# Kernel optimization log

Measured on AMD Instinct MI355X. Metric: run time of the kernel, lower is better.

The kernel has to match this reference:

```python
import jax, jax.numpy as jnp
import numpy as np

B, L, DIM, K = 2, 512, 128, 32
EPS = 1e-5  # torch LayerNorm default


def setup_inputs() -> dict:
    key = jax.random.key(0)
    ks = jax.random.split(key, 4)
    s = 1.0 / np.sqrt(DIM)
    s2 = 1.0 / np.sqrt(2 * DIM)
    return {
        "pair_repr": jax.random.normal(ks[0], (B, L, L, DIM), jnp.float32),
        "W_out": jax.random.uniform(ks[1], (DIM, DIM), jnp.float32, -s, s),
        "b_out": jnp.zeros((DIM,), jnp.float32),
        "W_in": jax.random.uniform(ks[2], (DIM, DIM), jnp.float32, -s, s),
        "b_in": jnp.zeros((DIM,), jnp.float32),
        "W_g": jax.random.uniform(ks[3], (2 * DIM, DIM), jnp.float32, -s2, s2),
        "b_g": jnp.zeros((DIM,), jnp.float32),
        "ln_w": jnp.ones((DIM,), jnp.float32),
        "ln_b": jnp.zeros((DIM,), jnp.float32),
    }


def reference(pair_repr, W_out, b_out, W_in, b_in, W_g, b_g, ln_w, ln_b):
    # Eval-mode deterministic sampling: torch.linspace(0, L-1, K).long()
    idx = jnp.floor(jnp.linspace(0.0, L - 1, K)).astype(jnp.int32)

    # Linear is affine, so mean(Linear(x)) == Linear(mean(x)); project after mean.
    out_mean = pair_repr[:, :, idx, :].mean(axis=2)          # (B, L, dim)
    out_agg = out_mean @ W_out + b_out                        # (B, L, dim)
    in_mean = pair_repr[:, idx, :, :].mean(axis=1)            # (B, L, dim)
    in_agg = in_mean @ W_in + b_in                            # (B, L, dim)

    # gate = sigmoid(Linear(cat(out_b, in_b))): split W_g to avoid materializing the 2*dim concat
    Wg_o, Wg_i = W_g[:DIM], W_g[DIM:]
    gate = jax.nn.sigmoid(
        (out_agg @ Wg_o)[:, :, None, :]
        + (in_agg @ Wg_i)[:, None, :, :]
        + b_g
    )                                                         # (B, L, L, dim)

    update = out_agg[:, :, None, :] + in_agg[:, None, :, :]   # (B, L, L, dim)
    x = pair_repr + gate * (update - pair_repr)

    # LayerNorm over last axis (biased variance, matching torch)
    mu = x.mean(axis=-1, keepdims=True)
    var = x.var(axis=-1, keepdims=True)
    return (x - mu) / jnp.sqrt(var + EPS) * ln_w + ln_b
```

## Files before the change

### kernel.cpp

```cpp
#include <hip/hip_runtime.h>
#include <hip/hip_bf16.h>

#define BB 2
#define LL 512
#define DIM 128
#define KK 32
#define EPSF 1e-5f

__global__ __launch_bounds__(DIM) void agg_gemm_kernel(
    const float* __restrict__ pair,
    const float* __restrict__ W_out, const float* __restrict__ b_out,
    const float* __restrict__ W_in,  const float* __restrict__ b_in,
    const float* __restrict__ W_g,
    float* __restrict__ agg,
    float* __restrict__ gpart)
{
    const int t    = threadIdx.x;
    const int bid  = blockIdx.x;
    const int path = bid >> 10;
    const int r    = bid & 1023;
    const int b    = r >> 9;
    const int q    = r & 511;

    __shared__ float sm[DIM];

    const float* base;
    long stride;
    if (path == 0) {
        base   = pair + ((long)(b * LL + q) * LL) * DIM + t;
        stride = DIM;
    } else {
        base   = pair + ((long)b * LL * LL) * DIM + (long)q * DIM + t;
        stride = (long)LL * DIM;
    }
    float acc = 0.f;
#pragma unroll
    for (int k = 0; k < KK; ++k) {
        const int jj = (k * (LL - 1)) / (KK - 1);
        acc += base[(long)jj * stride];
    }
    sm[t] = acc * (1.0f / KK);
    __syncthreads();

    const float* W    = (path == 0) ? W_out : W_in;
    const float* bias = (path == 0) ? b_out : b_in;
    float a = bias[t];
#pragma unroll 8
    for (int k = 0; k < DIM; ++k)
        a += sm[k] * W[k * DIM + t];
    __syncthreads();
    sm[t] = a;
    agg[(long)path * BB * LL * DIM + (long)r * DIM + t] = a;
    __syncthreads();

    const float* Wg = W_g + path * DIM * DIM;
    float g = 0.f;
#pragma unroll 8
    for (int k = 0; k < DIM; ++k)
        g += sm[k] * Wg[k * DIM + t];
    gpart[(long)path * BB * LL * DIM + (long)r * DIM + t] = g;
}

__device__ __forceinline__ void load8(const float* p, float* f) {
    const float4 a = reinterpret_cast<const float4*>(p)[0];
    const float4 b = reinterpret_cast<const float4*>(p)[1];
    f[0] = a.x; f[1] = a.y; f[2] = a.z; f[3] = a.w;
    f[4] = b.x; f[5] = b.y; f[6] = b.z; f[7] = b.w;
}

__global__ __launch_bounds__(256) void fuse_ln_kernel(
    const float* __restrict__ pair,
    const float* __restrict__ out_agg, const float* __restrict__ in_agg,
    const float* __restrict__ go,      const float* __restrict__ gi,
    const float* __restrict__ b_g, const float* __restrict__ ln_w,
    const float* __restrict__ ln_b,
    float* __restrict__ out)
{
    const int  tid    = threadIdx.x;
    const int  lane16 = tid & 15;
    const int  rloc   = tid >> 4;
    const long row    = (long)blockIdx.x * 16 + rloc;
    const int  j      = (int)(row & (LL - 1));
    const long bi     = row >> 9;
    const int  b      = (int)(bi >> 9);
    const int  e0     = lane16 * 8;
    const long bj     = (long)b * LL + j;

    float p[8], gof[8], gif[8], oaf[8], iaf[8], bg[8], lw[8], lb[8];
    load8(pair    + row * DIM + e0, p);
    load8(go      + bi  * DIM + e0, gof);
    load8(gi      + bj  * DIM + e0, gif);
    load8(out_agg + bi  * DIM + e0, oaf);
    load8(in_agg  + bj  * DIM + e0, iaf);
    load8(b_g  + e0, bg);
    load8(ln_w + e0, lw);
    load8(ln_b + e0, lb);

    float x[8];
    float sum = 0.f, ss = 0.f;
#pragma unroll
    for (int c = 0; c < 8; ++c) {
        const float z    = gof[c] + gif[c] + bg[c];
        const float gate = 1.0f / (1.0f + __builtin_amdgcn_exp2f(z * -1.442695041f));
        const float u    = oaf[c] + iaf[c];
        const float xv   = p[c] + gate * (u - p[c]);
        x[c] = xv;
        sum += xv;
        ss  += xv * xv;
    }

#pragma unroll
    for (int m = 1; m < 16; m <<= 1) {
        sum += __shfl_xor(sum, m);
        ss  += __shfl_xor(ss,  m);
    }
    const float mu   = sum * (1.0f / DIM);
    const float var  = ss * (1.0f / DIM) - mu * mu;
    const float rstd = rsqrtf(var + EPSF);

    float y[8];
#pragma unroll
    for (int c = 0; c < 8; ++c)
        y[c] = (x[c] - mu) * rstd * lw[c] + lb[c];

    float* op = out + row * DIM + e0;
    reinterpret_cast<float4*>(op)[0] = make_float4(y[0], y[1], y[2], y[3]);
    reinterpret_cast<float4*>(op)[1] = make_float4(y[4], y[5], y[6], y[7]);
}

extern "C" void kernel_launch(void* const* d_in, const int* in_sizes, int n_in,
                              void* d_out, int out_size, void* d_ws, size_t ws_size,
                              hipStream_t stream) {
    const float* pair  = (const float*)d_in[0];
    const float* W_out = (const float*)d_in[1];
    const float* b_out = (const float*)d_in[2];
    const float* W_in  = (const float*)d_in[3];
    const float* b_in  = (const float*)d_in[4];
    const float* W_g   = (const float*)d_in[5];
    const float* b_g   = (const float*)d_in[6];
    const float* ln_w  = (const float*)d_in[7];
    const float* ln_b  = (const float*)d_in[8];
    float* out = (float*)d_out;

    float* agg   = (float*)d_ws;
    float* gpart = agg + 2 * BB * LL * DIM;

    agg_gemm_kernel<<<2 * BB * LL, DIM, 0, stream>>>(
        pair, W_out, b_out, W_in, b_in, W_g, agg, gpart);

    const int rows_per_block = 16;
    fuse_ln_kernel<<<(BB * LL * LL) / rows_per_block, 256, 0, stream>>>(
        pair,
        agg,   agg   + BB * LL * DIM,
        gpart, gpart + BB * LL * DIM,
        b_g, ln_w, ln_b, out);
}
```

Baseline: 497.6 us.

## Make fused LayerNorm blocks persistent over half-rows with hoisted per-i vectors

The fused gate+LayerNorm kernel now gives each block half of one i-row (256 j values), looping over 16 rows per iteration. The per-i out_agg/gate vectors and the LN/bias parameters are loaded once per block instead of once per row. Element mapping changes to two interleaved float4 chunks so each warp's loads are contiguous, the reciprocal uses the fast rcp intrinsic, and launch bounds request 4 blocks per CU. The grid drops to 2048 blocks, which lowers parallelism slack. The kernel is dominated by HBM traffic, so the gain is likely small.

```diff
diff --git a/kernel.cpp b/kernel.cpp
--- a/kernel.cpp
+++ b/kernel.cpp
@@ -1,5 +1,4 @@
 #include <hip/hip_runtime.h>
-#include <hip/hip_bf16.h>
 
 #define BB 2
 #define LL 512
@@ -24,20 +23,21 @@
 
     __shared__ float sm[DIM];
 
-    const float* base;
-    long stride;
+    float acc = 0.f;
     if (path == 0) {
-        base   = pair + ((long)(b * LL + q) * LL) * DIM + t;
-        stride = DIM;
+        const float* base = pair + ((long)(b * LL + q) * LL) * DIM + t;
+#pragma unroll
+        for (int k = 0; k < KK; ++k) {
+            const int jj = (k * (LL - 1)) / (KK - 1);
+            acc += base[(long)jj * DIM];
+        }
     } else {
-        base   = pair + ((long)b * LL * LL) * DIM + (long)q * DIM + t;
-        stride = (long)LL * DIM;
-    }
-    float acc = 0.f;
+        const float* base = pair + (long)b * LL * LL * DIM + (long)q * DIM + t;
 #pragma unroll
-    for (int k = 0; k < KK; ++k) {
-        const int jj = (k * (LL - 1)) / (KK - 1);
-        acc += base[(long)jj * stride];
+        for (int k = 0; k < KK; ++k) {
+            const int jj = (k * (LL - 1)) / (KK - 1);
+            acc += base[(long)jj * (LL * DIM)];
+        }
     }
     sm[t] = acc * (1.0f / KK);
     __syncthreads();
@@ -61,14 +61,15 @@
     gpart[(long)path * BB * LL * DIM + (long)r * DIM + t] = g;
 }
 
-__device__ __forceinline__ void load8(const float* p, float* f) {
-    const float4 a = reinterpret_cast<const float4*>(p)[0];
-    const float4 b = reinterpret_cast<const float4*>(p)[1];
+__device__ __forceinline__ void load8c(const float* __restrict__ base,
+                                       int e0, int e1, float* f) {
+    const float4 a = *reinterpret_cast<const float4*>(base + e0);
+    const float4 b = *reinterpret_cast<const float4*>(base + e1);
     f[0] = a.x; f[1] = a.y; f[2] = a.z; f[3] = a.w;
     f[4] = b.x; f[5] = b.y; f[6] = b.z; f[7] = b.w;
 }
 
-__global__ __launch_bounds__(256) void fuse_ln_kernel(
+__global__ __launch_bounds__(256, 4) void fuse_ln_kernel(
     const float* __restrict__ pair,
     const float* __restrict__ out_agg, const float* __restrict__ in_agg,
     const float* __restrict__ go,      const float* __restrict__ gi,
@@ -76,56 +77,70 @@
     const float* __restrict__ ln_b,
     float* __restrict__ out)
 {
-    const int  tid    = threadIdx.x;
-    const int  lane16 = tid & 15;
-    const int  rloc   = tid >> 4;
-    const long row    = (long)blockIdx.x * 16 + rloc;
-    const int  j      = (int)(row & (LL - 1));
-    const long bi     = row >> 9;
-    const int  b      = (int)(bi >> 9);
-    const int  e0     = lane16 * 8;
-    const long bj     = (long)b * LL + j;
+    const int tid    = threadIdx.x;
+    const int lane16 = tid & 15;
+    const int rloc   = tid >> 4;
+    const int blk    = blockIdx.x;
+    const int half   = blk & 1;
+    const int bi     = blk >> 1;
+    const int b      = bi >> 9;
+    const int jbase  = half * (LL / 2);
 
-    float p[8], gof[8], gif[8], oaf[8], iaf[8], bg[8], lw[8], lb[8];
-    load8(pair    + row * DIM + e0, p);
-    load8(go      + bi  * DIM + e0, gof);
-    load8(gi      + bj  * DIM + e0, gif);
-    load8(out_agg + bi  * DIM + e0, oaf);
-    load8(in_agg  + bj  * DIM + e0, iaf);
-    load8(b_g  + e0, bg);
-    load8(ln_w + e0, lw);
-    load8(ln_b + e0, lb);
+    const int e0 = lane16 * 4;
+    const int e1 = 64 + lane16 * 4;
 
-    float x[8];
-    float sum = 0.f, ss = 0.f;
+    float gof[8], oaf[8], bg[8], lw[8], lb[8];
+    load8c(go      + (long)bi * DIM, e0, e1, gof);
+    load8c(out_agg + (long)bi * DIM, e0, e1, oaf);
+    load8c(b_g,  e0, e1, bg);
+    load8c(ln_w, e0, e1, lw);
+    load8c(ln_b, e0, e1, lb);
+
+    const long bL = (long)b * LL;
+
+#pragma unroll 2
+    for (int jt = 0; jt < (LL / 2) / 16; ++jt) {
+        const int  j   = jbase + jt * 16 + rloc;
+        const long row = (long)bi * LL + j;
+        const long bj  = bL + j;
+
+        float p[8], gif[8], iaf[8];
+        load8c(pair   + row * DIM, e0, e1, p);
+        load8c(gi     + bj  * DIM, e0, e1, gif);
+        load8c(in_agg + bj  * DIM, e0, e1, iaf);
+
+        float x[8];
+        float sum = 0.f, ss = 0.f;
 #pragma unroll
-    for (int c = 0; c < 8; ++c) {
-        const float z    = gof[c] + gif[c] + bg[c];
-        const float gate = 1.0f / (1.0f + __builtin_amdgcn_exp2f(z * -1.442695041f));
-        const float u    = oaf[c] + iaf[c];
-        const float xv   = p[c] + gate * (u - p[c]);
-        x[c] = xv;
-        sum += xv;
-        ss  += xv * xv;
-    }
+        for (int c = 0; c < 8; ++c) {
+            const float z    = gof[c] + gif[c] + bg[c];
+            const float e    = __builtin_amdgcn_exp2f(z * -1.442695041f);
+            const float gate = __builtin_amdgcn_rcpf(1.0f + e);
+            const float u    = oaf[c] + iaf[c];
+            const float xv   = p[c] + gate * (u - p[c]);
+            x[c] = xv;
+            sum += xv;
+            ss  += xv * xv;
+        }
 
 #pragma unroll
-    for (int m = 1; m < 16; m <<= 1) {
-        sum += __shfl_xor(sum, m);
-        ss  += __shfl_xor(ss,  m);
+        for (int m = 1; m < 16; m <<= 1) {
+            sum += __shfl_xor(sum, m);
+            ss  += __shfl_xor(ss,  m);
+        }
+        const float mu   = sum * (1.0f / DIM);
+        const float var  = ss * (1.0f / DIM) - mu * mu;
+        const float rstd = rsqrtf(var + EPSF);
+
+        float y[8];
+#pragma unroll
+        for (int c = 0; c < 8; ++c)
+            y[c] = (x[c] - mu) * rstd * lw[c] + lb[c];
+
+        float* op = out + row * DIM;
+        *reinterpret_cast<float4*>(op + e0) = make_float4(y[0], y[1], y[2], y[3]);
+        *reinterpret_cast<float4*>(op + e1) = make_float4(y[4], y[5], y[6], y[7]);
     }
-    const float mu   = sum * (1.0f / DIM);
-    const float var  = ss * (1.0f / DIM) - mu * mu;
-    const float rstd = rsqrtf(var + EPSF);
-
-    float y[8];
-#pragma unroll
-    for (int c = 0; c < 8; ++c)
-        y[c] = (x[c] - mu) * rstd * lw[c] + lb[c];
-
-    float* op = out + row * DIM + e0;
-    reinterpret_cast<float4*>(op)[0] = make_float4(y[0], y[1], y[2], y[3]);
-    reinterpret_cast<float4*>(op)[1] = make_float4(y[4], y[5], y[6], y[7]);
 }
 
 extern "C" void kernel_launch(void* const* d_in, const int* in_sizes, int n_in,
@@ -148,8 +163,7 @@
     agg_gemm_kernel<<<2 * BB * LL, DIM, 0, stream>>>(
         pair, W_out, b_out, W_in, b_in, W_g, agg, gpart);
 
-    const int rows_per_block = 16;
-    fuse_ln_kernel<<<(BB * LL * LL) / rows_per_block, 256, 0, stream>>>(
+    fuse_ln_kernel<<<2 * BB * LL, 256, 0, stream>>>(
         pair,
         agg,   agg   + BB * LL * DIM,
         gpart, gpart + BB * LL * DIM,
```

After: 484.7 us. 1.03x faster.
